# Performance work log

Measured on AMD Instinct MI355X. Metric: run time of the kernel, lower is better.

The kernel has to match this reference:

```python
import jax, jax.numpy as jnp
import numpy as np

B, N, C, H = 4, 2048, 1024, 16
HD = C // H  # head_dim = 64


def setup_inputs() -> dict:
    key = jax.random.key(0)
    ks = jax.random.split(key, 16)
    s = 0.02
    return {
        "x": jax.random.normal(ks[0], (B, N, C), dtype=jnp.float32),
        # qkv_proj: Linear(C, 3C): weight (3C, C), bias (3C,)
        "W_qkv": jax.random.normal(ks[1], (3 * C, C), dtype=jnp.float32) * s,
        "b_qkv": jax.random.normal(ks[2], (3 * C,), dtype=jnp.float32) * s,
        # out_proj: Linear(C, C)
        "W_out": jax.random.normal(ks[3], (C, C), dtype=jnp.float32) * s,
        "b_out": jax.random.normal(ks[4], (C,), dtype=jnp.float32) * s,
        # dynamically-reassigned position bias: shape (1, N, H, H) per the code's
        # (B, num_heads=N, seq_len=H, seq_len=H) score tensor
        "pos_bias": jax.random.normal(ks[5], (1, N, H, H), dtype=jnp.float32) * 0.01,
        # conv_proj: Linear(C, C)
        "W_cp": jax.random.normal(ks[6], (C, C), dtype=jnp.float32) * s,
        "b_cp": jax.random.normal(ks[7], (C,), dtype=jnp.float32) * s,
        # pointwise Conv1d(C, C, k=1): weight (C, C) after squeezing kernel dim
        "W_pw": jax.random.normal(ks[8], (C, C), dtype=jnp.float32) * s,
        "b_pw": jax.random.normal(ks[9], (C,), dtype=jnp.float32) * s,
        # depthwise Conv1d(C, C, k=3, groups=C): weight (C, 3)
        "W_dw": jax.random.normal(ks[10], (C, 3), dtype=jnp.float32) * s,
        "b_dw": jax.random.normal(ks[11], (C,), dtype=jnp.float32) * s,
        # token_wise_proj: Linear(C, C)
        "W_tw": jax.random.normal(ks[12], (C, C), dtype=jnp.float32) * s,
        "b_tw": jax.random.normal(ks[13], (C,), dtype=jnp.float32) * s,
    }


def reference(x, W_qkv, b_qkv, W_out, b_out, pos_bias, W_cp, b_cp,
              W_pw, b_pw, W_dw, b_dw, W_tw, b_tw) -> jnp.ndarray:
    Bx, Nx, Cx = x.shape
    scale = HD ** -0.5
    # qkv -> (B, N, H, 3*HD), chunk into q,k,v of (B, N, H, HD).
    # NOTE: faithful to the torch code, heads stay on axis 2; the matmul
    # contracts head_dim giving (B, N, H, H) scores (attention over heads).
    qkv = (x @ W_qkv.T + b_qkv).reshape(Bx, Nx, H, 3 * HD)
    q, k, v = jnp.split(qkv, 3, axis=-1)
    scores = jnp.einsum('bnhd,bngd->bnhg', q, k) * scale + pos_bias
    attn = jax.nn.softmax(scores, axis=-1)
    attn_out = jnp.einsum('bnhg,bngd->bnhd', attn, v).reshape(Bx, Nx, Cx)
    attn_out = attn_out @ W_out.T + b_out

    # Convolutional branch
    xc = x @ W_cp.T + b_cp          # conv_proj
    xc = xc @ W_pw.T + b_pw          # pointwise conv (k=1) == linear over channels
    xp = jnp.pad(xc, ((0, 0), (1, 1), (0, 0)))  # pad seq for k=3, padding=1
    xc = (xp[:, :-2] * W_dw[:, 0] + xp[:, 1:-1] * W_dw[:, 1]
          + xp[:, 2:] * W_dw[:, 2] + b_dw)      # depthwise conv
    xc = xc @ W_tw.T + b_tw          # token_wise_proj

    return attn_out + xc
```

## Files before the change

### kernel.cpp

```cpp
#include <hip/hip_runtime.h>
#include <hip/hip_bf16.h>
#include <stdint.h>

typedef __bf16 bf16_t;
typedef __attribute__((ext_vector_type(8))) __bf16 bf16x8;
typedef __attribute__((ext_vector_type(4))) __bf16 bf16x4;
typedef __attribute__((ext_vector_type(4))) float floatx4;
typedef __attribute__((ext_vector_type(4))) _Float16 half4_t;

#define GLDS16(g, l)                                                          \
  __builtin_amdgcn_global_load_lds(                                           \
      (const __attribute__((address_space(1))) void*)(g),                     \
      (__attribute__((address_space(3))) void*)(l), 16, 0, 0)

#define BAR8                                                                  \
  do {                                                                        \
    __builtin_amdgcn_s_barrier();                                             \
    __builtin_amdgcn_sched_barrier(0);                                        \
  } while (0)
#define VMCNT(n) asm volatile("s_waitcnt vmcnt(" #n ")")

template <int IT, int JT, typename OT>
__global__ __launch_bounds__(256) void gemm_bt(
    const bf16_t* __restrict__ A, const bf16_t* __restrict__ B,
    const float* __restrict__ bias, OT* __restrict__ C, int M, int N, int K) {
  constexpr int AROWS = 32 * IT;
  constexpr int BROWS = 32 * JT;
  constexpr int COLS = BROWS;
  constexpr int STAGE = (AROWS + BROWS) * 64;
  constexpr int EPI = (sizeof(OT) == 2) ? AROWS * COLS : 0;
  constexpr int SME = STAGE > EPI ? STAGE : EPI;
  __shared__ bf16_t sm[SME];
  bf16_t* As = sm;
  bf16_t* Bs = sm + AROWS * 64;

  const int tid = threadIdx.x;
  const int wave = tid >> 6;
  const int lane = tid & 63;
  const int quad = lane >> 4;
  const int l16 = lane & 15;
  const int m0 = blockIdx.x * AROWS;
  const int n0 = blockIdx.y * BROWS;
  const int wm = (wave >> 1) * (IT * 16);
  const int wn = (wave & 1) * (JT * 16);

  const int ra = wave * (8 * IT) + (lane >> 3);
  const int ga = ((lane & 7) ^ (ra & 7)) * 8;
  const int rb = wave * (8 * JT) + (lane >> 3);
  const int gb = ((lane & 7) ^ (rb & 7)) * 8;
  const bf16_t* Ab = A + (size_t)(m0 + ra) * K + ga;
  const bf16_t* Bb = B + (size_t)(n0 + rb) * K + gb;
  const int p0 = (quad ^ (l16 & 7)) * 8;

  floatx4 acc[IT][JT];
  const floatx4 zf = {0.f, 0.f, 0.f, 0.f};
#pragma unroll
  for (int i = 0; i < IT; ++i)
#pragma unroll
    for (int j = 0; j < JT; ++j) acc[i][j] = zf;

  for (int k0 = 0; k0 < K; k0 += 64) {
#pragma unroll
    for (int t = 0; t < IT; ++t)
      GLDS16(Ab + (size_t)(t * 8) * K + k0, As + (wave * (64 * IT) + t * 64) * 8);
#pragma unroll
    for (int t = 0; t < JT; ++t)
      GLDS16(Bb + (size_t)(t * 8) * K + k0, Bs + (wave * (64 * JT) + t * 64) * 8);
    __syncthreads();
#pragma unroll
    for (int ks = 0; ks < 2; ++ks) {
      const int ko = p0 ^ (ks * 32);
      bf16x8 af[IT], bfr[JT];
#pragma unroll
      for (int i = 0; i < IT; ++i)
        af[i] = *(const bf16x8*)(As + (wm + i * 16 + l16) * 64 + ko);
#pragma unroll
      for (int j = 0; j < JT; ++j)
        bfr[j] = *(const bf16x8*)(Bs + (wn + j * 16 + l16) * 64 + ko);
#pragma unroll
      for (int i = 0; i < IT; ++i)
#pragma unroll
        for (int j = 0; j < JT; ++j)
          acc[i][j] = __builtin_amdgcn_mfma_f32_16x16x32_bf16(
              bfr[j], af[i], acc[i][j], 0, 0, 0);
    }
    __syncthreads();
  }

  if constexpr (sizeof(OT) == 4) {
#pragma unroll
    for (int j = 0; j < JT; ++j) {
      const int colb = n0 + wn + j * 16 + quad * 4;
      floatx4 bv = zf;
      if (bias) bv = *(const floatx4*)(bias + colb);
#pragma unroll
      for (int i = 0; i < IT; ++i) {
        const int row = m0 + wm + i * 16 + l16;
        floatx4 v = acc[i][j] + bv;
        *(floatx4*)((float*)C + (size_t)row * N + colb) = v;
      }
    }
  } else {
    constexpr int SWZ = COLS / 32;
    constexpr int CPR = COLS / 8;
    constexpr int PASSES = (AROWS * CPR) / 256;
#pragma unroll
    for (int j = 0; j < JT; ++j) {
      const int colb = n0 + wn + j * 16 + quad * 4;
      floatx4 bv = zf;
      if (bias) bv = *(const floatx4*)(bias + colb);
      const int gcol = (wn + j * 16 + quad * 4) >> 2;
#pragma unroll
      for (int i = 0; i < IT; ++i) {
        const int rl = wm + i * 16 + l16;
        floatx4 v = acc[i][j] + bv;
        union {
          bf16_t b[4];
          uint2 u2;
        } pk;
        pk.b[0] = (bf16_t)v[0];
        pk.b[1] = (bf16_t)v[1];
        pk.b[2] = (bf16_t)v[2];
        pk.b[3] = (bf16_t)v[3];
        const int gsw = gcol ^ ((rl & 7) * SWZ);
        *(uint2*)(sm + rl * COLS + gsw * 4) = pk.u2;
      }
    }
    __syncthreads();
    bf16_t* Cb = (bf16_t*)C;
#pragma unroll
    for (int pass = 0; pass < PASSES; ++pass) {
      const int f = pass * 256 + tid;
      const int row = f / CPR;
      const int c16 = f % CPR;
      const int g0 = (2 * c16) ^ ((row & 7) * SWZ);
      uint4 v = *(const uint4*)(sm + row * COLS + g0 * 4);
      *(uint4*)(Cb + (size_t)(m0 + row) * N + n0 + c16 * 8) = v;
    }
  }
}

__global__ __launch_bounds__(512, 2) void gemm8p(
    const bf16_t* __restrict__ A, const bf16_t* __restrict__ B,
    const float* __restrict__ bias, bf16_t* __restrict__ C, int M, int N,
    int K) {
  __shared__ bf16_t sm8[65536];
  bf16_t* As = sm8;
  bf16_t* Bs = sm8 + 32768;

  const int tid = threadIdx.x;
  const int wave = tid >> 6, lane = tid & 63;
  const int l16 = lane & 15, quad = lane >> 4;
  const int wm = (wave >> 2) * 128, wn = (wave & 3) * 64;

  const int lin = blockIdx.y * gridDim.x + blockIdx.x;
  const int nwg = gridDim.x * gridDim.y;
  const int chunk = nwg >> 3;
  const int swz = (lin & 7) * chunk + (lin >> 3);
  const int bm = swz / gridDim.x;
  const int bn = swz % gridDim.x;
  const int m0 = bm << 8, n0 = bn << 8;

  const int srow = wave * 32 + (lane >> 2);
  const int kswz = ((lane & 3) * 8) ^ ((lane >> 5) << 4);
  const bf16_t* Ag = A + (size_t)(m0 + srow) * K + kswz;
  const bf16_t* Bg = B + (size_t)(n0 + srow) * K + kswz;
  const int sdst = wave * 1024;
  const size_t a16k = (size_t)K << 4;

  const int koe = (quad * 8) ^ ((l16 & 8) << 1);
  const int aoff = (wm + l16) * 32 + koe;
  const int boff = (wn + l16) * 32 + koe;

  floatx4 acc[8][4];
  const floatx4 zf = {0.f, 0.f, 0.f, 0.f};
#pragma unroll
  for (int i = 0; i < 8; ++i)
#pragma unroll
    for (int j = 0; j < 4; ++j) acc[i][j] = zf;

  bf16x8 af[4], bfr[4];

#define STG_A(buf, kh, TOFF)                                     \
  do {                                                           \
    bf16_t* _d = As + (buf)*16384 + (kh)*8192 + sdst;            \
    GLDS16(Ag + (TOFF) + (kh)*32, _d);                           \
    GLDS16(Ag + a16k + (TOFF) + (kh)*32, _d + 512);              \
  } while (0)
#define STG_B(buf, kh, TOFF)                                     \
  do {                                                           \
    bf16_t* _d = Bs + (buf)*16384 + (kh)*8192 + sdst;            \
    GLDS16(Bg + (TOFF) + (kh)*32, _d);                           \
    GLDS16(Bg + a16k + (TOFF) + (kh)*32, _d + 512);              \
  } while (0)
#define LDA4(buf, ks, mb)                                        \
  do {                                                           \
    const bf16_t* _p = As + (buf)*16384 + (ks)*8192 + aoff + (mb)*512; \
    af[0] = *(const bf16x8*)(_p);                                \
    af[1] = *(const bf16x8*)(_p + 512);                          \
    af[2] = *(const bf16x8*)(_p + 1024);                         \
    af[3] = *(const bf16x8*)(_p + 1536);                         \
  } while (0)
#define LDB4(buf, ks)                                            \
  do {                                                           \
    const bf16_t* _p = Bs + (buf)*16384 + (ks)*8192 + boff;      \
    bfr[0] = *(const bf16x8*)(_p);                               \
    bfr[1] = *(const bf16x8*)(_p + 512);                         \
    bfr[2] = *(const bf16x8*)(_p + 1024);                        \
    bfr[3] = *(const bf16x8*)(_p + 1536);                        \
  } while (0)
#define MFMA16(mb)                                               \
  do {                                                           \
    __builtin_amdgcn_s_setprio(1);                               \
    _Pragma("unroll") for (int _i = 0; _i < 4; ++_i)             \
        _Pragma("unroll") for (int _j = 0; _j < 4; ++_j)         \
            acc[(mb) + _i][_j] =                                 \
                __builtin_amdgcn_mfma_f32_16x16x32_bf16(         \
                    bfr[_j], af[_i], acc[(mb) + _i][_j], 0, 0, 0); \
    __builtin_amdgcn_s_setprio(0);                               \
  } while (0)

  STG_A(0, 0, 0);
  STG_A(0, 1, 0);
  STG_B(0, 0, 0);
  STG_B(0, 1, 0);
  STG_B(1, 0, 64);
  STG_A(1, 0, 64);
  STG_B(1, 1, 64);
  VMCNT(6);
  BAR8;

  const int NT = K >> 6;
  for (int it = 0; it < NT / 2 - 1; ++it) {
    LDA4(0, 0, 0); LDB4(0, 0); STG_A(1, 1, 64);            BAR8; MFMA16(0); BAR8;
    LDA4(0, 0, 4);             STG_B(0, 0, 128);           BAR8; MFMA16(4); BAR8;
    LDA4(0, 1, 0); LDB4(0, 1); STG_A(0, 0, 128);           BAR8; MFMA16(0); BAR8;
    LDA4(0, 1, 4);             STG_B(0, 1, 128); VMCNT(6); BAR8; MFMA16(4); BAR8;
    LDA4(1, 0, 0); LDB4(1, 0); STG_A(0, 1, 128);           BAR8; MFMA16(0); BAR8;
    LDA4(1, 0, 4);             STG_B(1, 0, 192);           BAR8; MFMA16(4); BAR8;
    LDA4(1, 1, 0); LDB4(1, 1); STG_A(1, 0, 192);           BAR8; MFMA16(0); BAR8;
    LDA4(1, 1, 4);             STG_B(1, 1, 192); VMCNT(6); BAR8; MFMA16(4); BAR8;
    Ag += 128;
    Bg += 128;
  }
  LDA4(0, 0, 0); LDB4(0, 0); STG_A(1, 1, 64); BAR8; MFMA16(0); BAR8;
  LDA4(0, 0, 4);                              BAR8; MFMA16(4); BAR8;
  LDA4(0, 1, 0); LDB4(0, 1);                  BAR8; MFMA16(0); BAR8;
  LDA4(0, 1, 4);             VMCNT(0);        BAR8; MFMA16(4); BAR8;
  LDA4(1, 0, 0); LDB4(1, 0);                  BAR8; MFMA16(0); BAR8;
  LDA4(1, 0, 4);                              BAR8; MFMA16(4); BAR8;
  LDA4(1, 1, 0); LDB4(1, 1);                  BAR8; MFMA16(0); BAR8;
  LDA4(1, 1, 4);                              BAR8; MFMA16(4); BAR8;

  const int crow_b = wm + l16;
#pragma unroll
  for (int nj = 0; nj < 4; ++nj) {
    const int colb = wn + nj * 16 + quad * 4;
    floatx4 bv = zf;
    if (bias) bv = *(const floatx4*)(bias + n0 + colb);
#pragma unroll
    for (int mi = 0; mi < 8; ++mi) {
      const int row = crow_b + mi * 16;
      floatx4 v = acc[mi][nj] + bv;
      union {
        bf16_t b[4];
        uint2 u2;
      } pk;
      pk.b[0] = (bf16_t)v[0];
      pk.b[1] = (bf16_t)v[1];
      pk.b[2] = (bf16_t)v[2];
      pk.b[3] = (bf16_t)v[3];
      const int cb = (colb * 2) ^ ((row & 31) << 4);
      *(uint2*)((char*)sm8 + row * 512 + cb) = pk.u2;
    }
  }
  __syncthreads();
#pragma unroll
  for (int pass = 0; pass < 16; ++pass) {
    const int flat = pass * 8192 + tid * 16;
    const int row = flat >> 9;
    const int cb = flat & 511;
    const int cbs = cb ^ ((row & 31) << 4);
    uint4 v = *(const uint4*)((char*)sm8 + row * 512 + cbs);
    *(uint4*)((char*)C + ((size_t)(m0 + row) * N + n0) * 2 + cb) = v;
  }
#undef STG_A
#undef STG_B
#undef LDA4
#undef LDB4
#undef MFMA16
}

__global__ __launch_bounds__(512, 2) void gemm8p2(
    const bf16_t* __restrict__ A, const bf16_t* __restrict__ B,
    const float* __restrict__ bias, float* __restrict__ C, int M, int N,
    int K) {
  __shared__ bf16_t sm2[49152];
  bf16_t* As = sm2;
  bf16_t* Bs = sm2 + 16384;

  const int tid = threadIdx.x;
  const int wave = tid >> 6, lane = tid & 63;
  const int l16 = lane & 15, quad = lane >> 4;
  const int wm = (wave >> 2) * 64, wn = (wave & 3) * 64;
  const int m0 = blockIdx.y << 7, n0 = blockIdx.x << 8;

  const int srA = wave * 16 + (lane >> 2);
  const int srB = wave * 32 + (lane >> 2);
  const int kswz = ((lane & 3) * 8) ^ ((lane >> 5) << 4);
  const bf16_t* Ag = A + (size_t)(m0 + srA) * K + kswz;
  const bf16_t* Bg = B + (size_t)(n0 + srB) * K + kswz;
  const size_t b16k = (size_t)K << 4;

  const int koe = (quad * 8) ^ ((l16 & 8) << 1);
  const int aoff = (wm + l16) * 32 + koe;
  const int boff = (wn + l16) * 32 + koe;

  floatx4 acc[4][4];
  const floatx4 zf = {0.f, 0.f, 0.f, 0.f};
#pragma unroll
  for (int i = 0; i < 4; ++i)
#pragma unroll
    for (int j = 0; j < 4; ++j) acc[i][j] = zf;

  bf16x8 af[4], bfr[4];

#define SA2(buf, kh, TOFF)                                                 \
  GLDS16(Ag + (TOFF) + (kh)*32, As + (buf)*8192 + (kh)*4096 + wave * 512)
#define SB2(buf, kh, TOFF)                                                 \
  do {                                                                     \
    bf16_t* _d = Bs + (buf)*16384 + (kh)*8192 + wave * 1024;               \
    GLDS16(Bg + (TOFF) + (kh)*32, _d);                                     \
    GLDS16(Bg + b16k + (TOFF) + (kh)*32, _d + 512);                        \
  } while (0)
#define LD2(buf, kh)                                                       \
  do {                                                                     \
    const bf16_t* _pa = As + (buf)*8192 + (kh)*4096 + aoff;                \
    const bf16_t* _pb = Bs + (buf)*16384 + (kh)*8192 + boff;               \
    _Pragma("unroll") for (int _i = 0; _i < 4; ++_i)                       \
        af[_i] = *(const bf16x8*)(_pa + _i * 512);                         \
    _Pragma("unroll") for (int _j = 0; _j < 4; ++_j)                       \
        bfr[_j] = *(const bf16x8*)(_pb + _j * 512);                        \
  } while (0)
#define MM2                                                                \
  do {                                                                     \
    __builtin_amdgcn_s_setprio(1);                                         \
    _Pragma("unroll") for (int _i = 0; _i < 4; ++_i)                       \
        _Pragma("unroll") for (int _j = 0; _j < 4; ++_j)                   \
            acc[_i][_j] = __builtin_amdgcn_mfma_f32_16x16x32_bf16(         \
                bfr[_j], af[_i], acc[_i][_j], 0, 0, 0);                    \
    __builtin_amdgcn_s_setprio(0);                                         \
  } while (0)

  SA2(0, 0, 0);
  SB2(0, 0, 0);
  SA2(0, 1, 0);
  SB2(0, 1, 0);
  SA2(1, 0, 64);
  SB2(1, 0, 64);
  VMCNT(3);
  BAR8;

  const int NT = K >> 6;
  for (int it = 0; it < NT / 2 - 1; ++it) {
    LD2(0, 0); SA2(1, 1, 64);  SB2(1, 1, 64);            BAR8; MM2; BAR8;
    LD2(0, 1); SA2(0, 0, 128); SB2(0, 0, 128); VMCNT(3); BAR8; MM2; BAR8;
    LD2(1, 0); SA2(0, 1, 128); SB2(0, 1, 128);           BAR8; MM2; BAR8;
    LD2(1, 1); SA2(1, 0, 192); SB2(1, 0, 192); VMCNT(3); BAR8; MM2; BAR8;
    Ag += 128;
    Bg += 128;
  }
  LD2(0, 0); SA2(1, 1, 64); SB2(1, 1, 64); BAR8; MM2; BAR8;
  LD2(0, 1); VMCNT(0);                     BAR8; MM2; BAR8;
  LD2(1, 0);                               BAR8; MM2; BAR8;
  LD2(1, 1);                                     MM2;

#pragma unroll
  for (int j = 0; j < 4; ++j) {
    const int colb = n0 + wn + j * 16 + quad * 4;
    floatx4 bv = zf;
    if (bias) bv = *(const floatx4*)(bias + colb);
#pragma unroll
    for (int i = 0; i < 4; ++i) {
      const int row = m0 + wm + i * 16 + l16;
      floatx4 v = acc[i][j] + bv;
      *(floatx4*)(C + (size_t)row * N + colb) = v;
    }
  }
#undef SA2
#undef SB2
#undef LD2
#undef MM2
}

__global__ __launch_bounds__(256) void prep2_k(
    const float* __restrict__ x, bf16_t* __restrict__ x_bf,
    const float* __restrict__ Wqkv, bf16_t* __restrict__ Wbig1,
    const float* __restrict__ Wpw, bf16_t* __restrict__ Wpw_bf,
    const float* __restrict__ Wout, const float* __restrict__ Wtw,
    bf16_t* __restrict__ Wbig2, const float* __restrict__ bqkv,
    float* __restrict__ bias1, const float* __restrict__ bout,
    const float* __restrict__ btw, float* __restrict__ bias2,
    const float* __restrict__ Wcp, bf16_t* __restrict__ WcpT,
    const float* __restrict__ bcp, const float* __restrict__ bpw) {
  __shared__ float t[32][33];
  const int b = blockIdx.x, tid = threadIdx.x;
  auto cvt4 = [](const float* in, bf16_t* out, int i) {
    floatx4 v = ((const floatx4*)in)[i];
    bf16x4 o;
    o[0] = (bf16_t)v[0];
    o[1] = (bf16_t)v[1];
    o[2] = (bf16_t)v[2];
    o[3] = (bf16_t)v[3];
    ((bf16x4*)out)[i] = o;
  };
  if (b < 8192) {
    cvt4(x, x_bf, b * 256 + tid);
  } else if (b < 11264) {
    cvt4(Wqkv, Wbig1, (b - 8192) * 256 + tid);
  } else if (b < 12288) {
    cvt4(Wpw, Wpw_bf, (b - 11264) * 256 + tid);
  } else if (b < 14336) {
    const bool second = b >= 13312;
    int i = (b - (second ? 13312 : 12288)) * 256 + tid;
    floatx4 v = ((const floatx4*)(second ? Wtw : Wout))[i];
    bf16x4 o;
    o[0] = (bf16_t)v[0];
    o[1] = (bf16_t)v[1];
    o[2] = (bf16_t)v[2];
    o[3] = (bf16_t)v[3];
    int row = i >> 8, c4 = i & 255;
    *(bf16x4*)(Wbig2 + (size_t)row * 2048 + (second ? 1024 : 0) + c4 * 4) = o;
  } else if (b < 14339) {
    int i = (b - 14336) * 256 + tid;
    if (i < 768) ((floatx4*)bias1)[i] = ((const floatx4*)bqkv)[i];
  } else if (b == 14339) {
    ((floatx4*)bias2)[tid] =
        ((const floatx4*)bout)[tid] + ((const floatx4*)btw)[tid];
  } else if (b < 15364) {
    const int tb = b - 14340;
    const int bx = (tb & 31) * 32, by = (tb >> 5) * 32;
    const int tx = tid & 31, ty = tid >> 5;
#pragma unroll
    for (int iq = 0; iq < 4; ++iq)
      t[ty + iq * 8][tx] = Wcp[(size_t)(by + ty + iq * 8) * 1024 + bx + tx];
    __syncthreads();
#pragma unroll
    for (int iq = 0; iq < 4; ++iq)
      WcpT[(size_t)(bx + ty + iq * 8) * 1024 + by + tx] =
          (bf16_t)t[tx][ty + iq * 8];
  } else {
    const int row = (b - 15364) * 4 + (tid >> 6);
    const int l = tid & 63;
    const float* wr = Wpw + (size_t)row * 1024;
    float s = 0.f;
    for (int j = l; j < 1024; j += 64) s += wr[j] * bcp[j];
#pragma unroll
    for (int o = 32; o > 0; o >>= 1) s += __shfl_down(s, o);
    if (l == 0) bias1[3072 + row] = s + bpw[row];
  }
}

static __device__ inline void exp8(uint32_t w0, uint32_t w1, uint32_t w2,
                                   uint32_t w3, float* f) {
  f[0] = __uint_as_float(w0 << 16);
  f[1] = __uint_as_float(w0 & 0xffff0000u);
  f[2] = __uint_as_float(w1 << 16);
  f[3] = __uint_as_float(w1 & 0xffff0000u);
  f[4] = __uint_as_float(w2 << 16);
  f[5] = __uint_as_float(w2 & 0xffff0000u);
  f[6] = __uint_as_float(w3 << 16);
  f[7] = __uint_as_float(w3 & 0xffff0000u);
}

__global__ __launch_bounds__(256) void mid_k(const bf16_t* __restrict__ G1,
                                             const float* __restrict__ pos,
                                             const float* __restrict__ Wdw,
                                             const float* __restrict__ bdw,
                                             bf16_t* __restrict__ Mid) {
  __shared__ bf16_t ost[4][16 * 68];
  const int tid = threadIdx.x;
  if (blockIdx.x < 2048) {
    const int wave = tid >> 6, lane = tid & 63;
    const int p = blockIdx.x * 4 + wave;
    const int l16 = lane & 15, quad = lane >> 4;
    const bf16_t* row = G1 + (size_t)p * 4096;
    const bf16_t* qb = row + l16 * 192 + quad * 8;

    bf16x8 q0 = *(const bf16x8*)(qb);
    bf16x8 q1 = *(const bf16x8*)(qb + 32);
    bf16x8 k0 = *(const bf16x8*)(qb + 64);
    bf16x8 k1 = *(const bf16x8*)(qb + 96);
    floatx4 S = {0.f, 0.f, 0.f, 0.f};
    S = __builtin_amdgcn_mfma_f32_16x16x32_bf16(k0, q0, S, 0, 0, 0);
    S = __builtin_amdgcn_mfma_f32_16x16x32_bf16(k1, q1, S, 0, 0, 0);

    const floatx4 pb = *(const floatx4*)(pos + (size_t)(p & 2047) * 256 +
                                         l16 * 16 + quad * 4);
    float v[4];
#pragma unroll
    for (int r = 0; r < 4; ++r) v[r] = S[r] * 0.125f + pb[r];

    float m = fmaxf(fmaxf(v[0], v[1]), fmaxf(v[2], v[3]));
    m = fmaxf(m, __shfl_xor(m, 16));
    m = fmaxf(m, __shfl_xor(m, 32));
    float e[4], sum = 0.f;
#pragma unroll
    for (int r = 0; r < 4; ++r) {
      e[r] = __expf(v[r] - m);
      sum += e[r];
    }
    sum += __shfl_xor(sum, 16);
    sum += __shfl_xor(sum, 32);
    const float inv = 1.0f / sum;
    half4_t pa;
#pragma unroll
    for (int r = 0; r < 4; ++r) pa[r] = (_Float16)(e[r] * inv);

    const bf16_t* vb_base = row + 128 + l16;
    const floatx4 zf = {0.f, 0.f, 0.f, 0.f};
    floatx4 o[4];
#pragma unroll
    for (int t = 0; t < 4; ++t) {
      half4_t vb;
#pragma unroll
      for (int j = 0; j < 4; ++j)
        vb[j] = (_Float16)(float)vb_base[(quad * 4 + j) * 192 + t * 16];
      o[t] = __builtin_amdgcn_mfma_f32_16x16x16f16(pa, vb, zf, 0, 0, 0);
    }

    bf16_t* ow = ost[wave];
#pragma unroll
    for (int r = 0; r < 4; ++r)
#pragma unroll
      for (int t = 0; t < 4; ++t)
        ow[(quad * 4 + r) * 68 + t * 16 + l16] = (bf16_t)o[t][r];
    const int h2 = lane >> 2, m4 = lane & 3;
    const bf16_t* srcp = ow + h2 * 68 + m4 * 16;
    uint2 a0 = *(const uint2*)(srcp);
    uint2 a1 = *(const uint2*)(srcp + 4);
    uint2 a2 = *(const uint2*)(srcp + 8);
    uint2 a3 = *(const uint2*)(srcp + 12);
    uint4 s0 = {a0.x, a0.y, a1.x, a1.y};
    uint4 s1 = {a2.x, a2.y, a3.x, a3.y};
    uint4* dst = (uint4*)(Mid + (size_t)p * 2048 + h2 * 64 + m4 * 16);
    dst[0] = s0;
    dst[1] = s1;
  } else {
    const bf16_t* in = G1 + 3072;
    bf16_t* out = Mid + 1024;
    const int item = (blockIdx.x - 2048) * 256 + tid;
    const int cc = item & 127, rowg = item >> 7;
    const int c0 = cc * 8;
    float w0[8], w1[8], w2[8], bb[8];
#pragma unroll
    for (int c = 0; c < 8; ++c) {
      w0[c] = Wdw[(c0 + c) * 3];
      w1[c] = Wdw[(c0 + c) * 3 + 1];
      w2[c] = Wdw[(c0 + c) * 3 + 2];
      bb[c] = bdw[c0 + c];
    }
#pragma unroll
    for (int jr = 0; jr < 4; ++jr) {
      const int tt = rowg * 4 + jr;
      const int n = tt & 2047;
      const bf16_t* ip = in + (size_t)tt * 4096 + c0;
      const uint4 z4 = {0, 0, 0, 0};
      uint4 um = (n > 0) ? *(const uint4*)(ip - 4096) : z4;
      uint4 uc = *(const uint4*)(ip);
      uint4 up = (n < 2047) ? *(const uint4*)(ip + 4096) : z4;
      float fm[8], fc[8], fp[8];
      exp8(um.x, um.y, um.z, um.w, fm);
      exp8(uc.x, uc.y, uc.z, uc.w, fc);
      exp8(up.x, up.y, up.z, up.w, fp);
      union {
        bf16_t b[8];
        uint4 u;
      } pk;
#pragma unroll
      for (int c = 0; c < 8; ++c)
        pk.b[c] =
            (bf16_t)(bb[c] + fm[c] * w0[c] + fc[c] * w1[c] + fp[c] * w2[c]);
      *(uint4*)(out + (size_t)tt * 2048 + c0) = pk.u;
    }
  }
}

extern "C" void kernel_launch(void* const* d_in, const int* in_sizes, int n_in,
                              void* d_out, int out_size, void* d_ws,
                              size_t ws_size, hipStream_t stream) {
  (void)in_sizes; (void)n_in; (void)out_size; (void)ws_size;
  const float* x = (const float*)d_in[0];
  const float* Wqkv = (const float*)d_in[1];
  const float* bqkv = (const float*)d_in[2];
  const float* Wout = (const float*)d_in[3];
  const float* bout = (const float*)d_in[4];
  const float* pos = (const float*)d_in[5];
  const float* Wcp = (const float*)d_in[6];
  const float* bcp = (const float*)d_in[7];
  const float* Wpw = (const float*)d_in[8];
  const float* bpw = (const float*)d_in[9];
  const float* Wdw = (const float*)d_in[10];
  const float* bdw = (const float*)d_in[11];
  const float* Wtw = (const float*)d_in[12];
  const float* btw = (const float*)d_in[13];
  float* out = (float*)d_out;

  char* ws = (char*)d_ws;
  const size_t MB = 1024ull * 1024ull;
  bf16_t* x_bf = (bf16_t*)(ws + 0);
  bf16_t* Wbig1 = (bf16_t*)(ws + 16 * MB);
  bf16_t* WcpT = (bf16_t*)(ws + 24 * MB);
  bf16_t* Wpw_bf = (bf16_t*)(ws + 26 * MB);
  bf16_t* Mid = (bf16_t*)(ws + 0);
  bf16_t* Wbig2 = (bf16_t*)(ws + 32 * MB);
  float* bias1 = (float*)(ws + 36 * MB);
  float* bias2 = (float*)(ws + 36 * MB + 65536);
  bf16_t* G1out = (bf16_t*)(ws + 37 * MB);

  prep2_k<<<15620, 256, 0, stream>>>(x, x_bf, Wqkv, Wbig1, Wpw, Wpw_bf, Wout,
                                     Wtw, Wbig2, bqkv, bias1, bout, btw, bias2,
                                     Wcp, WcpT, bcp, bpw);

  gemm_bt<2, 2, bf16_t><<<dim3(16, 16), 256, 0, stream>>>(
      Wpw_bf, WcpT, nullptr, Wbig1 + (size_t)3072 * 1024, 1024, 1024, 1024);

  gemm8p<<<dim3(16, 32), 512, 0, stream>>>(x_bf, Wbig1, bias1, G1out, 8192,
                                           4096, 1024);

  mid_k<<<3072, 256, 0, stream>>>(G1out, pos, Wdw, bdw, Mid);

  gemm8p2<<<dim3(4, 64), 512, 0, stream>>>(Mid, Wbig2, bias2, out, 8192, 1024,
                                           2048);
}
```

Measured before the change: 275.7 us.

## Split QKV GEMM launch in two, use asm barriers, stage V through LDS

The big QKV/conv GEMM is launched as two half-M grids through a new row-offset argument instead of one launch. The pipelined barriers become a bare inline-asm s_barrier with a memory clobber, so the sched_barrier that pinned instruction order is gone. In the attention-over-heads kernel, V rows are loaded with coalesced 16-byte loads into LDS and then gathered from there, replacing strided scalar global loads. The split adds launch overhead and may hurt tail balance, and the looser barrier lets the compiler reorder more freely around the MFMA blocks.

```diff
diff --git a/kernel.cpp b/kernel.cpp
--- a/kernel.cpp
+++ b/kernel.cpp
@@ -19,6 +19,7 @@
     __builtin_amdgcn_sched_barrier(0);                                        \
   } while (0)
 #define VMCNT(n) asm volatile("s_waitcnt vmcnt(" #n ")")
+#define BARD asm volatile("s_barrier" ::: "memory")
 
 template <int IT, int JT, typename OT>
 __global__ __launch_bounds__(256) void gemm_bt(
@@ -143,7 +144,7 @@
 __global__ __launch_bounds__(512, 2) void gemm8p(
     const bf16_t* __restrict__ A, const bf16_t* __restrict__ B,
     const float* __restrict__ bias, bf16_t* __restrict__ C, int M, int N,
-    int K) {
+    int K, int moff) {
   __shared__ bf16_t sm8[65536];
   bf16_t* As = sm8;
   bf16_t* Bs = sm8 + 32768;
@@ -159,7 +160,7 @@
   const int swz = (lin & 7) * chunk + (lin >> 3);
   const int bm = swz / gridDim.x;
   const int bn = swz % gridDim.x;
-  const int m0 = bm << 8, n0 = bn << 8;
+  const int m0 = (bm << 8) + moff, n0 = bn << 8;
 
   const int srow = wave * 32 + (lane >> 2);
   const int kswz = ((lane & 3) * 8) ^ ((lane >> 5) << 4);
@@ -359,20 +360,20 @@
   SA2(1, 0, 64);
   SB2(1, 0, 64);
   VMCNT(3);
-  BAR8;
+  BARD;
 
   const int NT = K >> 6;
   for (int it = 0; it < NT / 2 - 1; ++it) {
-    LD2(0, 0); SA2(1, 1, 64);  SB2(1, 1, 64);            BAR8; MM2; BAR8;
-    LD2(0, 1); SA2(0, 0, 128); SB2(0, 0, 128); VMCNT(3); BAR8; MM2; BAR8;
-    LD2(1, 0); SA2(0, 1, 128); SB2(0, 1, 128);           BAR8; MM2; BAR8;
-    LD2(1, 1); SA2(1, 0, 192); SB2(1, 0, 192); VMCNT(3); BAR8; MM2; BAR8;
+    LD2(0, 0); SA2(1, 1, 64);  SB2(1, 1, 64);            BARD; MM2; BARD;
+    LD2(0, 1); SA2(0, 0, 128); SB2(0, 0, 128); VMCNT(3); BARD; MM2; BARD;
+    LD2(1, 0); SA2(0, 1, 128); SB2(0, 1, 128);           BARD; MM2; BARD;
+    LD2(1, 1); SA2(1, 0, 192); SB2(1, 0, 192); VMCNT(3); BARD; MM2; BARD;
     Ag += 128;
     Bg += 128;
   }
-  LD2(0, 0); SA2(1, 1, 64); SB2(1, 1, 64); BAR8; MM2; BAR8;
-  LD2(0, 1); VMCNT(0);                     BAR8; MM2; BAR8;
-  LD2(1, 0);                               BAR8; MM2; BAR8;
+  LD2(0, 0); SA2(1, 1, 64); SB2(1, 1, 64); BARD; MM2; BARD;
+  LD2(0, 1); VMCNT(0);                     BARD; MM2; BARD;
+  LD2(1, 0);                               BARD; MM2; BARD;
   LD2(1, 1);                                     MM2;
 
 #pragma unroll
@@ -487,6 +488,16 @@
     const bf16_t* row = G1 + (size_t)p * 4096;
     const bf16_t* qb = row + l16 * 192 + quad * 8;
 
+    bf16_t* vs = ost[wave];
+    {
+      const int g = lane >> 2, dq = lane & 3;
+      const bf16_t* vsrc = row + g * 192 + 128 + dq * 16;
+      bf16x8 v0 = *(const bf16x8*)(vsrc);
+      bf16x8 v1 = *(const bf16x8*)(vsrc + 8);
+      *(bf16x8*)(vs + g * 68 + dq * 16) = v0;
+      *(bf16x8*)(vs + g * 68 + dq * 16 + 8) = v1;
+    }
+
     bf16x8 q0 = *(const bf16x8*)(qb);
     bf16x8 q1 = *(const bf16x8*)(qb + 32);
     bf16x8 k0 = *(const bf16x8*)(qb + 64);
@@ -517,7 +528,6 @@
 #pragma unroll
     for (int r = 0; r < 4; ++r) pa[r] = (_Float16)(e[r] * inv);
 
-    const bf16_t* vb_base = row + 128 + l16;
     const floatx4 zf = {0.f, 0.f, 0.f, 0.f};
     floatx4 o[4];
 #pragma unroll
@@ -525,7 +535,7 @@
       half4_t vb;
 #pragma unroll
       for (int j = 0; j < 4; ++j)
-        vb[j] = (_Float16)(float)vb_base[(quad * 4 + j) * 192 + t * 16];
+        vb[j] = (_Float16)(float)vs[(quad * 4 + j) * 68 + t * 16 + l16];
       o[t] = __builtin_amdgcn_mfma_f32_16x16x16f16(pa, vb, zf, 0, 0, 0);
     }
 
@@ -625,8 +635,10 @@
   gemm_bt<2, 2, bf16_t><<<dim3(16, 16), 256, 0, stream>>>(
       Wpw_bf, WcpT, nullptr, Wbig1 + (size_t)3072 * 1024, 1024, 1024, 1024);
 
-  gemm8p<<<dim3(16, 32), 512, 0, stream>>>(x_bf, Wbig1, bias1, G1out, 8192,
-                                           4096, 1024);
+  gemm8p<<<dim3(16, 16), 512, 0, stream>>>(x_bf, Wbig1, bias1, G1out, 8192,
+                                           4096, 1024, 0);
+  gemm8p<<<dim3(16, 16), 512, 0, stream>>>(x_bf, Wbig1, bias1, G1out, 8192,
+                                           4096, 1024, 4096);
 
   mid_k<<<3072, 256, 0, stream>>>(G1out, pos, Wdw, bdw, Mid);
 
```

Result: no change. 271.0 us (-1.7%).
